# Kernel tuning notes

Measured on AMD Instinct MI355X. Metric: run time of the kernel, lower is better.

## Reference

```python
import jax, jax.numpy as jnp
import numpy as np

B, H, W, N = 8, 384, 384, 96
STEPSZ = 0.1; ALPHA = 0.01; BETA = 0.01; STD = 1.0
NSTEPS = 50; NSTEPS_W = 10; DMAX = 15.0; EXTGRADFAC = 10.0

def make_gauss_edge_fltr(std):
    # Gaussian-derivative edge filters, one per spatial dim: [2,1,k,k]
    r = int(np.ceil(3 * std)); t = np.arange(-r, r + 1, dtype=np.float32)
    g = np.exp(-t * t / (2 * std * std)); g /= g.sum()
    dg = -t / (std * std) * np.exp(-t * t / (2 * std * std)); dg /= np.abs(dg).sum()
    fy = np.outer(dg, g)   # d/drow
    fx = np.outer(g, dg)   # d/dcol
    return np.stack([fy, fx])[:, None].astype(np.float32)

def setup_inputs() -> dict:
    key = jax.random.key(0)
    k1, k2 = jax.random.split(key, 2)
    pred_dmap = jax.random.normal(k1, (B, 1, H, W), jnp.float32)
    nodes = jax.random.uniform(k2, (B, N, 2), jnp.float32)
    nodes = nodes * jnp.array([H - 1.0, W - 1.0], jnp.float32)
    nodes = jnp.sort(nodes, axis=1)  # roughly monotone chain -> path-like snake
    widths = jnp.ones((B, N), jnp.float32) * 3.0
    fltr = jnp.asarray(make_gauss_edge_fltr(STD))
    return {"pred_dmap": pred_dmap, "nodes": nodes, "widths": widths, "fltr": fltr}

def grad_im(x, fltr):
    # x: [B,1,H,W], fltr: [2,1,k,k] -> [B,2,H,W]
    return jax.lax.conv_general_dilated(x, fltr, (1, 1), 'SAME',
                                        dimension_numbers=('NCHW', 'OIHW', 'NCHW'))

def interp(img, pts):
    # bilinear sample: img [C,H,W], pts [N,2] (row,col) -> [N,C]
    C, Hh, Ww = img.shape
    y = jnp.clip(pts[:, 0], 0.0, Hh - 1.0); x = jnp.clip(pts[:, 1], 0.0, Ww - 1.0)
    y0 = jnp.floor(y).astype(jnp.int32); x0 = jnp.floor(x).astype(jnp.int32)
    y1 = jnp.minimum(y0 + 1, Hh - 1); x1 = jnp.minimum(x0 + 1, Ww - 1)
    wy = y - y0; wx = x - x0
    v00 = img[:, y0, x0]; v01 = img[:, y0, x1]
    v10 = img[:, y1, x0]; v11 = img[:, y1, x1]
    v = v00 * (1 - wy) * (1 - wx) + v01 * (1 - wy) * wx + v10 * wy * (1 - wx) + v11 * wy * wx
    return v.T

def d2_open(x):
    # second difference with replicated endpoints (open snake)
    xp = jnp.concatenate([x[:1], x, x[-1:]], 0)
    return xp[:-2] - 2 * xp[1:-1] + xp[2:]

def snake_one(nodes, widths, g, gw):
    # explicit active-contour iterations on node positions
    def pstep(x, _):
        fext = interp(g, x)                       # [N,2] external force
        d2 = d2_open(x); d4 = d2_open(d2)
        return x + STEPSZ * (ALPHA * d2 - BETA * d4 + fext), None
    x, _ = jax.lax.scan(pstep, nodes, None, length=NSTEPS)
    # unit normals from central-difference tangents
    t = jnp.concatenate([x[1:2] - x[0:1], 0.5 * (x[2:] - x[:-2]), x[-1:] - x[-2:-1]], 0)
    n = jnp.stack([-t[:, 1], t[:, 0]], 1)
    n = n / (jnp.linalg.norm(n, axis=1, keepdims=True) + 1e-6)
    def wstep(w, _):
        gp = interp(gw, x + w[:, None] * n); gm = interp(gw, x - w[:, None] * n)
        f = 0.5 * (jnp.sum(gp * n, 1) - jnp.sum(gm * n, 1))
        return jnp.maximum(w + STEPSZ * f, 0.5), None
    w, _ = jax.lax.scan(wstep, widths, None, length=NSTEPS_W)
    return x, w

def render(x, w):
    # distance-to-ribbon map, clipped at DMAX; only [HW,S] intermediates
    ys, xs = jnp.meshgrid(jnp.arange(H, dtype=jnp.float32),
                          jnp.arange(W, dtype=jnp.float32), indexing='ij')
    P = jnp.stack([ys.ravel(), xs.ravel()], 1)          # [HW,2]
    a = x[:-1]; ab = x[1:] - a                          # [S,2]
    denom = jnp.sum(ab * ab, 1) + 1e-8                  # [S]
    dotpa = P @ ab.T - jnp.sum(a * ab, 1)               # [HW,S] = (P-a).ab
    t = jnp.clip(dotpa / denom, 0.0, 1.0)
    pa2 = jnp.sum(P * P, 1)[:, None] - 2 * (P @ a.T) + jnp.sum(a * a, 1)  # |P-a|^2
    d = jnp.sqrt(jnp.maximum(pa2 - 2 * t * dotpa + t * t * denom, 0.0))
    ws = 0.5 * (w[:-1] + w[1:])                         # per-segment width
    dmap = jnp.min(jnp.maximum(d - ws, 0.0), axis=1)
    return jnp.minimum(dmap, DMAX).reshape(H, W)

def reference(pred_dmap, nodes, widths, fltr):
    gimg = grad_im(pred_dmap, fltr) * EXTGRADFAC          # [B,2,H,W]
    gimgW = grad_im(jnp.abs(pred_dmap), fltr) * EXTGRADFAC
    def per_sample(nd, wd, g, gw):
        x, w = snake_one(nd, wd, g, gw)
        return render(x, w)
    dm = jax.vmap(per_sample)(nodes, widths, gimg, gimgW)[:, None]  # [B,1,H,W]
    dm = jax.lax.stop_gradient(dm)   # snake_dm.detach() in the original
    return jnp.mean((pred_dmap - dm) ** 2)
```

## Files before the change

kernel.cpp:

```cpp
#include <hip/hip_runtime.h>
#include <math.h>

#define BB   8
#define HH   384
#define WW   384
#define NN   96
#define HWSZ (HH * WW)
#define NSEG (NN - 1)
#define SEGF 12
#define SEGPAD 1152
#define DMAXV 15.0f
#define ROWS_PER_BLK 12
#define NCHUNK (HH / ROWS_PER_BLK)
#define CROWS 12
#define CBANDS (HH / CROWS)
#define MAGICU 0x9E3779B9u

typedef unsigned long long u64;
typedef unsigned int u32;

__device__ inline void st_pair(float* p, float lo, float hi)
{
    u64 v = ((u64)__float_as_uint(hi) << 32) | (u64)__float_as_uint(lo);
    __hip_atomic_store((u64*)p, v, __ATOMIC_RELAXED, __HIP_MEMORY_SCOPE_AGENT);
}

__device__ inline float ld_f32_coh(const float* p)
{
    u32 v = __hip_atomic_load((u32*)p, __ATOMIC_RELAXED, __HIP_MEMORY_SCOPE_AGENT);
    return __uint_as_float(v);
}

#define WAIT_ALL() asm volatile("s_waitcnt vmcnt(0) lgkmcnt(0)" ::: "memory")

__device__ inline void lds_barrier()
{
    asm volatile("s_waitcnt lgkmcnt(0)" ::: "memory");
    __builtin_amdgcn_sched_barrier(0);
    __builtin_amdgcn_s_barrier();
    __builtin_amdgcn_sched_barrier(0);
}

__device__ inline void load_taps(const float* __restrict__ fltr,
                                 float* __restrict__ sg, float* __restrict__ sdg)
{
    int tid = threadIdx.x;
    if (tid < 7) {
        float s = 0.f;
#pragma unroll
        for (int i = 0; i < 7; ++i) s += fabsf(fltr[i * 7 + tid]);
        sg[tid] = s;
    } else if (tid < 14) {
        int r = tid - 7;
        float s = 0.f;
#pragma unroll
        for (int j = 0; j < 7; ++j) s += fltr[r * 7 + j];
        sdg[r] = s;
    }
    __syncthreads();
}

__global__ __launch_bounds__(384) void conv_fused(
    const float* __restrict__ pred, const float* __restrict__ fltr,
    float2* __restrict__ g2, float2* __restrict__ gw2)
{
    __shared__ float sg[7], sdg[7];
    load_taps(fltr, sg, sdg);

    int blk = blockIdx.x;
    int b = blk & 7;
    int band = blk >> 3;
    int y0 = band * CROWS;
    int x = threadIdx.x;
    const float* pb = pred + (size_t)b * HWSZ;
    bool xin = (x >= 3) && (x < WW - 3);

    float hg[7], hd[7], hga[7], hda[7];

#pragma unroll
    for (int q = 0; q < CROWS + 6; ++q) {
        float vg = 0.f, vd = 0.f, vga = 0.f, vda = 0.f;
        int r = y0 + q - 3;
        if (r >= 0 && r < HH) {
            const float* row = pb + r * WW;
            if (xin) {
#pragma unroll
                for (int k = 0; k < 7; ++k) {
                    float v  = row[x + k - 3];
                    float av = fabsf(v);
                    vg  = fmaf(v,  sg[k],  vg);
                    vd  = fmaf(v,  sdg[k], vd);
                    vga = fmaf(av, sg[k],  vga);
                    vda = fmaf(av, sdg[k], vda);
                }
            } else {
#pragma unroll
                for (int k = 0; k < 7; ++k) {
                    int ix = x + k - 3;
                    float v  = (ix >= 0 && ix < WW) ? row[ix] : 0.f;
                    float av = fabsf(v);
                    vg  = fmaf(v,  sg[k],  vg);
                    vd  = fmaf(v,  sdg[k], vd);
                    vga = fmaf(av, sg[k],  vga);
                    vda = fmaf(av, sdg[k], vda);
                }
            }
        }
        hg[q % 7] = vg; hd[q % 7] = vd; hga[q % 7] = vga; hda[q % 7] = vda;

        if (q >= 6) {
            int y = y0 + q - 6;
            float o0 = 0.f, o1 = 0.f, o2 = 0.f, o3 = 0.f;
#pragma unroll
            for (int j = 0; j < 7; ++j) {
                int s = (q - 6 + j) % 7;
                o0 = fmaf(hg[s],  sdg[j], o0);
                o1 = fmaf(hd[s],  sg[j],  o1);
                o2 = fmaf(hga[s], sdg[j], o2);
                o3 = fmaf(hda[s], sg[j],  o3);
            }
            size_t gi = (size_t)b * HWSZ + (size_t)y * WW + x;
            g2[gi]  = make_float2(o0 * 10.f, o1 * 10.f);
            gw2[gi] = make_float2(o2 * 10.f, o3 * 10.f);
        }
    }
}

__device__ inline float2 bilin2i(const float2* __restrict__ img, float py, float px)
{
    float y = fminf(fmaxf(py, 0.0f), (float)(HH - 1));
    float x = fminf(fmaxf(px, 0.0f), (float)(WW - 1));
    int y0 = (int)floorf(y);
    int x0 = (int)floorf(x);
    int y1 = min(y0 + 1, HH - 1);
    bool xedge = (x0 + 1 > WW - 1);
    float wy = y - (float)y0;
    float wx = x - (float)x0;
    float4 r0 = *(const float4*)(img + y0 * WW + x0);
    float4 r1 = *(const float4*)(img + y1 * WW + x0);
    float2 v00 = make_float2(r0.x, r0.y);
    float2 v01 = xedge ? v00 : make_float2(r0.z, r0.w);
    float2 v10 = make_float2(r1.x, r1.y);
    float2 v11 = xedge ? v10 : make_float2(r1.z, r1.w);
    float w00 = (1.f - wy) * (1.f - wx);
    float w01 = (1.f - wy) * wx;
    float w10 = wy * (1.f - wx);
    float w11 = wy * wx;
    return make_float2(v00.x * w00 + v01.x * w01 + v10.x * w10 + v11.x * w11,
                       v00.y * w00 + v01.y * w01 + v10.y * w10 + v11.y * w11);
}

__device__ inline void write_seg_wt(float* __restrict__ r,
                                    float py, float px, float qy, float qx, float wseg)
{
    float aby = qy - py, abx = qx - px;
    float denom = aby * aby + abx * abx + 1e-8f;
    float aab = py * aby + px * abx;
    float aa  = py * py + px * px;
    float reach = DMAXV + wseg;
    st_pair(r + 0,  py,  px);
    st_pair(r + 2,  aby, abx);
    st_pair(r + 4,  aab, denom);
    st_pair(r + 6,  1.0f / denom, aa);
    st_pair(r + 8,  wseg, fminf(py, qy) - reach);
    st_pair(r + 10, fmaxf(py, qy) + reach, 0.f);
}

__global__ __launch_bounds__(384) void snake_render(
    const float* __restrict__ pred, const float* __restrict__ nodes,
    const float* __restrict__ widths,
    const float* __restrict__ g2f, const float* __restrict__ gw2f,
    float* __restrict__ segs, u64* __restrict__ pflag,
    u32* __restrict__ segflag, float* __restrict__ out)
{
    __shared__ float ss[NSEG * SEGF];
    __shared__ float2 posb[2][NN];
    __shared__ float  wbuf[NN];
    __shared__ int slo, shi;
    __shared__ float swsum[6];

    int blk = blockIdx.x;
    int b   = blk & 7;
    int band = blk >> 3;
    int t = threadIdx.x;

    int y0r = band * ROWS_PER_BLK;
    const float* pb = pred + (size_t)b * HWSZ + (size_t)y0r * WW + t;
    float pv[ROWS_PER_BLK];
#pragma unroll
    for (int ry = 0; ry < ROWS_PER_BLK; ++ry) pv[ry] = pb[ry * WW];

    if (t == 0) { slo = NSEG; shi = -1; }

    if (blk < 8) {
        const float2* gb  = (const float2*)g2f  + (size_t)b * HWSZ;
        const float2* gwb = (const float2*)gw2f + (size_t)b * HWSZ;
        int wv = t >> 6, ln = t & 63;
        int n  = wv * 48 + ln;
        bool act = (wv < 2) && (ln < 48);
        bool n0f = (n == 0), nlf = (n == NN - 1);

        float py = 0.f, px = 0.f;
        float4 r0 = make_float4(0.f, 0.f, 0.f, 0.f), r1 = r0;
        float wy = 0.f, wx = 0.f;
        bool xedge = false;

        if (act) {
            float2 p0 = *(const float2*)(nodes + (size_t)(b * NN + n) * 2);
            py = p0.x; px = p0.y;
            posb[0][n] = p0;
            float yc = fminf(fmaxf(py, 0.0f), (float)(HH - 1));
            float xc = fminf(fmaxf(px, 0.0f), (float)(WW - 1));
            int y0i = (int)floorf(yc);
            int x0i = (int)floorf(xc);
            int y1i = min(y0i + 1, HH - 1);
            xedge = (x0i + 1 > WW - 1);
            wy = yc - (float)y0i;
            wx = xc - (float)x0i;
            r0 = *(const float4*)(gb + y0i * WW + x0i);
            r1 = *(const float4*)(gb + y1i * WW + x0i);
        }
        lds_barrier();

        for (int s = 0; s < 50; ++s) {
            const float2* pcur = posb[s & 1];
            float2* pnxt = posb[(s & 1) ^ 1];
            if (act) {
                float2 xm1 = pcur[max(n - 1, 0)];
                float2 xp1 = pcur[min(n + 1, NN - 1)];
                float2 xm2 = pcur[max(n - 2, 0)];
                float2 xp2 = pcur[min(n + 2, NN - 1)];

                float d2m_y = xm2.x - 2.f * xm1.x + py;
                float d2c_y = xm1.x - 2.f * py + xp1.x;
                float d2p_y = py - 2.f * xp1.x + xp2.x;
                float d2m_x = xm2.y - 2.f * xm1.y + px;
                float d2c_x = xm1.y - 2.f * px + xp1.y;
                float d2p_x = px - 2.f * xp1.y + xp2.y;
                d2m_y = n0f ? d2c_y : d2m_y;
                d2m_x = n0f ? d2c_x : d2m_x;
                d2p_y = nlf ? d2c_y : d2p_y;
                d2p_x = nlf ? d2c_x : d2p_x;
                float d4_y = d2m_y - 2.f * d2c_y + d2p_y;
                float d4_x = d2m_x - 2.f * d2c_x + d2p_x;

                float2 v00 = make_float2(r0.x, r0.y);
                float2 v01 = xedge ? v00 : make_float2(r0.z, r0.w);
                float2 v10 = make_float2(r1.x, r1.y);
                float2 v11 = xedge ? v10 : make_float2(r1.z, r1.w);
                float w00 = (1.f - wy) * (1.f - wx);
                float w01 = (1.f - wy) * wx;
                float w10 = wy * (1.f - wx);
                float w11 = wy * wx;
                float fy = v00.x * w00 + v01.x * w01 + v10.x * w10 + v11.x * w11;
                float fx = v00.y * w00 + v01.y * w01 + v10.y * w10 + v11.y * w11;

                py += 0.1f * (0.01f * d2c_y - 0.01f * d4_y + fy);
                px += 0.1f * (0.01f * d2c_x - 0.01f * d4_x + fx);

                float yc = fminf(fmaxf(py, 0.0f), (float)(HH - 1));
                float xc = fminf(fmaxf(px, 0.0f), (float)(WW - 1));
                int y0i = (int)floorf(yc);
                int x0i = (int)floorf(xc);
                int y1i = min(y0i + 1, HH - 1);
                xedge = (x0i + 1 > WW - 1);
                wy = yc - (float)y0i;
                wx = xc - (float)x0i;
                r0 = *(const float4*)(gb + y0i * WW + x0i);
                r1 = *(const float4*)(gb + y1i * WW + x0i);

                pnxt[n] = make_float2(py, px);
            }
            lds_barrier();
        }

        float ny_ = 0.f, nx_ = 0.f, wn = 0.f;
        if (act) {
            float2 xm1 = posb[0][max(n - 1, 0)];
            float2 xp1 = posb[0][min(n + 1, NN - 1)];
            float ty, tx;
            if (n0f)      { ty = xp1.x - py;  tx = xp1.y - px; }
            else if (nlf) { ty = py - xm1.x;  tx = px - xm1.y; }
            else          { ty = 0.5f * (xp1.x - xm1.x); tx = 0.5f * (xp1.y - xm1.y); }

            float nn0 = -tx, nn1 = ty;
            float nrm = sqrtf(nn0 * nn0 + nn1 * nn1) + 1e-6f;
            ny_ = nn0 / nrm; nx_ = nn1 / nrm;

            wn = widths[b * NN + n];
            for (int s = 0; s < 10; ++s) {
                float2 gp = bilin2i(gwb, py + wn * ny_, px + wn * nx_);
                float2 gm = bilin2i(gwb, py - wn * ny_, px - wn * nx_);
                float fw = 0.5f * ((gp.x * ny_ + gp.y * nx_) - (gm.x * ny_ + gm.y * nx_));
                wn = fmaxf(wn + 0.1f * fw, 0.5f);
            }
            wbuf[n] = wn;
        }
        __syncthreads();

        if (act && n < NSEG) {
            float2 q = posb[0][n + 1];
            float wq = wbuf[n + 1];
            write_seg_wt(segs + (size_t)b * SEGPAD + (size_t)n * SEGF,
                         py, px, q.x, q.y, 0.5f * (wn + wq));
        }
        WAIT_ALL();
        __syncthreads();
        if (t == 0)
            __hip_atomic_store(&segflag[b], MAGICU,
                               __ATOMIC_RELAXED, __HIP_MEMORY_SCOPE_AGENT);
    } else {
        {
            int pband = band - 1;
            const int NV4 = (2 * HWSZ) / 4;
            const float4* s0 = (const float4*)(g2f  + (size_t)b * 2 * HWSZ);
            const float4* s1 = (const float4*)(gw2f + (size_t)b * 2 * HWSZ);
            float acc = 0.f;
            for (int i = pband * 384 + t; i < NV4; i += 31 * 384) {
                float4 a = s0[i];
                float4 c = s1[i];
                acc += a.x + c.x;
            }
            asm volatile("" :: "v"(acc));
        }
        if (t == 0) {
            while (__hip_atomic_load(&segflag[b],
                                     __ATOMIC_RELAXED, __HIP_MEMORY_SCOPE_AGENT) != MAGICU)
                __builtin_amdgcn_s_sleep(8);
            asm volatile("" ::: "memory");
        }
    }

    __syncthreads();

    {
        int y0 = y0r;
        const float* sb = segs + (size_t)b * SEGPAD;
        for (int j = t; j < NSEG * SEGF; j += 384)
            ss[j] = ld_f32_coh(sb + j);
        __syncthreads();

        float cy0 = (float)y0, cy1 = (float)(y0 + ROWS_PER_BLK - 1);
        if (t < NSEG) {
            float ylo = ss[t * SEGF + 9];
            float yhi = ss[t * SEGF + 10];
            if (yhi >= cy0 && ylo <= cy1) {
                atomicMin(&slo, t);
                atomicMax(&shi, t);
            }
        }
        __syncthreads();
        int lo = slo, hi = shi;

        float px = (float)t;
        float px2 = px * px;
        float minv[ROWS_PER_BLK];
#pragma unroll
        for (int r = 0; r < ROWS_PER_BLK; ++r) minv[r] = DMAXV;

        for (int si = lo; si <= hi; ++si) {
            const float* r = ss + si * SEGF;
            float ax = r[1], abx = r[3], ws = r[8];
            float bxe = ax + abx;
            float reach = DMAXV + ws + 0.01f;
            if (px < fminf(ax, bxe) - reach || px > fmaxf(ax, bxe) + reach) continue;

            float ay = r[0], aby = r[2];
            float aab = r[4], denom = r[5], invd = r[6], aa = r[7];
            float dotpa_b = fmaf(px, abx, -aab);
            float pa2_b   = fmaf(px, -2.0f * ax, px2 + aa);
#pragma unroll
            for (int ry = 0; ry < ROWS_PER_BLK; ++ry) {
                float py = (float)(y0 + ry);
                float dotpa = fmaf(py, aby, dotpa_b);
                float tt = fminf(fmaxf(dotpa * invd, 0.0f), 1.0f);
                float pa2 = fmaf(py, fmaf(py, 1.0f, -2.0f * ay), pa2_b);
                float d2 = fmaf(tt, fmaf(tt, denom, -2.0f * dotpa), pa2);
                float d = sqrtf(fmaxf(d2, 0.0f));
                float v = fmaxf(d - ws, 0.0f);
                minv[ry] = fminf(minv[ry], v);
            }
        }

        float sq = 0.f;
#pragma unroll
        for (int ry = 0; ry < ROWS_PER_BLK; ++ry) {
            float diff = pv[ry] - minv[ry];
            sq = fmaf(diff, diff, sq);
        }

#pragma unroll
        for (int off = 32; off > 0; off >>= 1) sq += __shfl_down(sq, off, 64);
        if ((t & 63) == 0) swsum[t >> 6] = sq;
        __syncthreads();
        if (t == 0) {
            float tot = swsum[0] + swsum[1] + swsum[2] + swsum[3] + swsum[4] + swsum[5];
            u64 pvv = ((u64)MAGICU << 32) | (u64)__float_as_uint(tot);
            __hip_atomic_store(&pflag[blk], pvv,
                               __ATOMIC_RELAXED, __HIP_MEMORY_SCOPE_AGENT);
        }
    }

    if (blk == 8) {
        __syncthreads();
        float v = 0.f;
        if (t < 256) {
            u64 pvv = __hip_atomic_load(&pflag[t], __ATOMIC_RELAXED,
                                        __HIP_MEMORY_SCOPE_AGENT);
            while ((u32)(pvv >> 32) != MAGICU) {
                __builtin_amdgcn_s_sleep(4);
                pvv = __hip_atomic_load(&pflag[t], __ATOMIC_RELAXED,
                                        __HIP_MEMORY_SCOPE_AGENT);
            }
            v = __uint_as_float((u32)pvv);
        }
#pragma unroll
        for (int off = 32; off > 0; off >>= 1) v += __shfl_down(v, off, 64);
        if ((t & 63) == 0) swsum[t >> 6] = v;
        __syncthreads();
        if (t == 0) {
            float tot = swsum[0] + swsum[1] + swsum[2] + swsum[3] + swsum[4] + swsum[5];
            out[0] = tot * (1.0f / (float)(BB * HWSZ));
        }
    }
}

extern "C" void kernel_launch(void* const* d_in, const int* in_sizes, int n_in,
                              void* d_out, int out_size, void* d_ws, size_t ws_size,
                              hipStream_t stream)
{
    const float* pred   = (const float*)d_in[0];
    const float* nodes  = (const float*)d_in[1];
    const float* widths = (const float*)d_in[2];
    const float* fltr   = (const float*)d_in[3];
    float* out = (float*)d_out;

    float* ws   = (float*)d_ws;
    float* g2   = ws;
    float* gw2  = g2 + (size_t)2 * BB * HWSZ;
    float* segs = gw2 + (size_t)2 * BB * HWSZ;
    float* tail = segs + (size_t)BB * SEGPAD + 256;
    u64* pflag = (u64*)tail;
    u32* segflag = (u32*)(pflag + 256);

    conv_fused<<<BB * CBANDS, 384, 0, stream>>>(pred, fltr,
                                                (float2*)g2, (float2*)gw2);
    snake_render<<<BB * NCHUNK, 384, 0, stream>>>(pred, nodes, widths, g2, gw2,
                                                  segs, pflag, segflag, out);
}
```

Measured before the change: 122.1 us.

## Warm gradient images into the L2 of the XCD running each snake block

Each snake block reads its hardware XCC id and publishes it in a workspace map. Non-snake blocks then prefetch gradient images only for the snake samples running on their own XCD, instead of the sample with their own batch index. The idle waves of the snake block also stream its own gradient images during the iteration loop. The goal is to make the snake's data-dependent bilinear gathers hit a local L2. The cost is extra spin-waiting on the map and extra memory traffic. The map is never cleared, so a stale tag from an earlier call could send prefetch to the wrong XCD.

Result: slower. 213.1 us (+74.6%).

```diff
diff --git a/kernel.cpp b/kernel.cpp
--- a/kernel.cpp
+++ b/kernel.cpp
@@ -15,6 +15,9 @@
 #define CROWS 12
 #define CBANDS (HH / CROWS)
 #define MAGICU 0x9E3779B9u
+#define XTAG   0xA5A50000u
+#define NV4    (2 * HWSZ / 4)
+#define XCCID_IMM 63508
 
 typedef unsigned long long u64;
 typedef unsigned int u32;
@@ -171,7 +174,8 @@
     const float* __restrict__ widths,
     const float* __restrict__ g2f, const float* __restrict__ gw2f,
     float* __restrict__ segs, u64* __restrict__ pflag,
-    u32* __restrict__ segflag, float* __restrict__ out)
+    u32* __restrict__ segflag, u32* __restrict__ xcdmap,
+    float* __restrict__ out)
 {
     __shared__ float ss[NSEG * SEGF];
     __shared__ float2 posb[2][NN];
@@ -193,8 +197,16 @@
     if (t == 0) { slo = NSEG; shi = -1; }
 
     if (blk < 8) {
+        if (t == 0) {
+            u32 xid = __builtin_amdgcn_s_getreg(XCCID_IMM) & 0xFu;
+            __hip_atomic_store(&xcdmap[b], XTAG | xid,
+                               __ATOMIC_RELAXED, __HIP_MEMORY_SCOPE_AGENT);
+        }
+
         const float2* gb  = (const float2*)g2f  + (size_t)b * HWSZ;
         const float2* gwb = (const float2*)gw2f + (size_t)b * HWSZ;
+        const float4* g4b  = (const float4*)(g2f  + (size_t)b * 2 * HWSZ);
+        const float4* gw4b = (const float4*)(gw2f + (size_t)b * 2 * HWSZ);
         int wv = t >> 6, ln = t & 63;
         int n  = wv * 48 + ln;
         bool act = (wv < 2) && (ln < 48);
@@ -204,6 +216,7 @@
         float4 r0 = make_float4(0.f, 0.f, 0.f, 0.f), r1 = r0;
         float wy = 0.f, wx = 0.f;
         bool xedge = false;
+        float waccum = 0.f;
 
         if (act) {
             float2 p0 = *(const float2*)(nodes + (size_t)(b * NN + n) * 2);
@@ -270,9 +283,23 @@
                 r1 = *(const float4*)(gb + y1i * WW + x0i);
 
                 pnxt[n] = make_float2(py, px);
+            } else if (wv >= 2) {
+                int wt = t - 128;
+                int base = s * 24;
+#pragma unroll
+                for (int k = 0; k < 24; ++k) {
+                    int i = (base + k) * 256 + wt;
+                    if (i < 2 * NV4) {
+                        const float4* src = (i < NV4) ? (g4b + i)
+                                                      : (gw4b + (i - NV4));
+                        float4 a = *src;
+                        waccum += a.x;
+                    }
+                }
             }
             lds_barrier();
         }
+        asm volatile("" :: "v"(waccum));
 
         float ny_ = 0.f, nx_ = 0.f, wn = 0.f;
         if (act) {
@@ -311,17 +338,28 @@
                                __ATOMIC_RELAXED, __HIP_MEMORY_SCOPE_AGENT);
     } else {
         {
-            int pband = band - 1;
-            const int NV4 = (2 * HWSZ) / 4;
-            const float4* s0 = (const float4*)(g2f  + (size_t)b * 2 * HWSZ);
-            const float4* s1 = (const float4*)(gw2f + (size_t)b * 2 * HWSZ);
-            float acc = 0.f;
-            for (int i = pband * 384 + t; i < NV4; i += 31 * 384) {
-                float4 a = s0[i];
-                float4 c = s1[i];
-                acc += a.x + c.x;
-            }
-            asm volatile("" :: "v"(acc));
+            u32 myx = __builtin_amdgcn_s_getreg(XCCID_IMM) & 0xFu;
+            int rank = blk % 31;
+            int warmed = 0;
+            for (int ib = 0; ib < 8 && warmed < 2; ++ib) {
+                u32 m;
+                do {
+                    m = __hip_atomic_load(&xcdmap[ib], __ATOMIC_RELAXED,
+                                          __HIP_MEMORY_SCOPE_AGENT);
+                    if ((m & 0xFFFF0000u) != XTAG) __builtin_amdgcn_s_sleep(1);
+                } while ((m & 0xFFFF0000u) != XTAG);
+                if ((m & 0xFu) != myx) continue;
+                ++warmed;
+                const float4* s0 = (const float4*)(g2f  + (size_t)ib * 2 * HWSZ);
+                const float4* s1 = (const float4*)(gw2f + (size_t)ib * 2 * HWSZ);
+                float acc = 0.f;
+                for (int i = rank * 384 + t; i < NV4; i += 31 * 384) {
+                    float4 a = s0[i];
+                    float4 c = s1[i];
+                    acc += a.x + c.x;
+                }
+                asm volatile("" :: "v"(acc));
+            }
         }
         if (t == 0) {
             while (__hip_atomic_load(&segflag[b],
@@ -442,9 +480,11 @@
     float* tail = segs + (size_t)BB * SEGPAD + 256;
     u64* pflag = (u64*)tail;
     u32* segflag = (u32*)(pflag + 256);
+    u32* xcdmap  = segflag + 8;
 
     conv_fused<<<BB * CBANDS, 384, 0, stream>>>(pred, fltr,
                                                 (float2*)g2, (float2*)gw2);
     snake_render<<<BB * NCHUNK, 384, 0, stream>>>(pred, nodes, widths, g2, gw2,
-                                                  segs, pflag, segflag, out);
-}
+                                                  segs, pflag, segflag, xcdmap,
+                                                  out);
+}
```
